# Performance work log

Measured on AMD Instinct MI355X. Metric: run time of the kernel, lower is better.

The kernel has to match this reference:

```python
import jax, jax.numpy as jnp
import numpy as np

L, B, S, CACHE = 2, 1, 2048, 2048
H, HKV, D, DM, FF, V = 16, 8, 128, 2048, 8192, 32000
EPS = 1e-6
ROPE_BASE = 10000.0


def setup_inputs() -> dict:
    key = jax.random.key(0)
    ks = jax.random.split(key, 18)
    std = 0.02
    r = lambda k, shape: (jax.random.normal(k, shape, dtype=jnp.float32) * std)
    return {
        "input_ids": jax.random.randint(ks[0], (B, S), 0, V),
        "embed": r(ks[1], (V, DM)),
        "Wq": r(ks[2], (L, DM, H * D)),
        "Wk": r(ks[3], (L, DM, HKV * D)),
        "Wv": r(ks[4], (L, DM, HKV * D)),
        "Wo": r(ks[5], (L, H * D, DM)),
        "Wg": r(ks[6], (L, DM, FF)),
        "Wu": r(ks[7], (L, DM, FF)),
        "Wd": r(ks[8], (L, FF, DM)),
        "ln1": jnp.ones((L, DM), jnp.float32),
        "ln2": jnp.ones((L, DM), jnp.float32),
        "final_norm": jnp.ones((DM,), jnp.float32),
        "lm_head": r(ks[9], (DM, V)),
        "k_cache": jax.random.normal(ks[10], (L, B, H, CACHE, D), jnp.float32),
        "v_cache": jax.random.normal(ks[11], (L, B, H, CACHE, D), jnp.float32),
    }


def rms_norm(x, w):
    return x * jax.lax.rsqrt(jnp.mean(x * x, axis=-1, keepdims=True) + EPS) * w


def apply_rope(x, pos):
    # x: [B,H,T,D], pos: [T]
    inv_freq = 1.0 / (ROPE_BASE ** (jnp.arange(0, D, 2, dtype=jnp.float32) / D))
    f = pos[:, None].astype(jnp.float32) * inv_freq[None, :]  # [T, D/2]
    emb = jnp.concatenate([f, f], axis=-1)                    # [T, D]
    cos, sin = jnp.cos(emb), jnp.sin(emb)
    rot = jnp.concatenate([-x[..., D // 2:], x[..., : D // 2]], axis=-1)
    return x * cos + rot * sin


def decoder_forward(input_ids, embed, Wq, Wk, Wv, Wo, Wg, Wu, Wd,
                    ln1, ln2, final_norm, lm_head, k_cache, v_cache):
    h = embed[input_ids]  # [B,S,DM]
    T = CACHE + S
    q_pos = jnp.arange(CACHE, CACHE + S)
    k_pos = jnp.arange(T)
    # causal mask: query i (global pos CACHE+i) attends keys <= CACHE+i
    mask = k_pos[None, :] <= (CACHE + jnp.arange(S))[:, None]  # [S,T]
    scale = 1.0 / np.sqrt(D)

    def layer(h, params):
        wq, wk, wv, wo, wg, wu, wd, l1, l2, kc, vc = params
        x = rms_norm(h, l1)
        q = (x @ wq).reshape(B, S, H, D).transpose(0, 2, 1, 3)     # [B,H,S,D]
        k = (x @ wk).reshape(B, S, HKV, D).transpose(0, 2, 1, 3)   # [B,HKV,S,D]
        v = (x @ wv).reshape(B, S, HKV, D).transpose(0, 2, 1, 3)
        k = jnp.repeat(k, H // HKV, axis=1)                        # repeat_kv
        v = jnp.repeat(v, H // HKV, axis=1)
        k = jnp.concatenate([kc, k], axis=2)                       # [B,H,T,D]
        v = jnp.concatenate([vc, v], axis=2)
        q = apply_rope(q, q_pos)
        k = apply_rope(k, k_pos)
        scores = jnp.einsum('bhqd,bhkd->bhqk', q, k) * scale
        scores = jnp.where(mask, scores, jnp.float32(-1e30))
        attn = jax.nn.softmax(scores, axis=-1)
        o = jnp.einsum('bhqk,bhkd->bhqd', attn, v)
        o = o.transpose(0, 2, 1, 3).reshape(B, S, H * D) @ wo
        h = h + o
        x = rms_norm(h, l2)
        h = h + (jax.nn.silu(x @ wg) * (x @ wu)) @ wd
        return h, None

    h, _ = jax.lax.scan(layer, h, (Wq, Wk, Wv, Wo, Wg, Wu, Wd, ln1, ln2, k_cache, v_cache))
    h = rms_norm(h, final_norm)
    return (h @ lm_head).astype(jnp.float32)  # logits [B,S,V]


def reference(input_ids, embed, Wq, Wk, Wv, Wo, Wg, Wu, Wd,
              ln1, ln2, final_norm, lm_head, k_cache, v_cache):
    return decoder_forward(input_ids, embed, Wq, Wk, Wv, Wo, Wg, Wu, Wd,
                           ln1, ln2, final_norm, lm_head, k_cache, v_cache)
```

## Files before the change

kernel.cpp:

```cpp
#include <hip/hip_runtime.h>

typedef __attribute__((ext_vector_type(8))) short bfrag8;
typedef __attribute__((ext_vector_type(4))) short bfrag4;
typedef __attribute__((ext_vector_type(4))) float facc4;

#define DEV_INLINE __device__ __forceinline__

DEV_INLINE short f2bf(float f) {
    union { float f; unsigned u; } x; x.f = f;
    unsigned r = (x.u + 0x7FFFu + ((x.u >> 16) & 1u)) >> 16;
    return (short)r;
}

DEV_INLINE float bf2f(short s) {
    union { unsigned u; float f; } x;
    x.u = ((unsigned)(unsigned short)s) << 16;
    return x.f;
}

DEV_INLINE unsigned pack_bf2(float a, float b) {
    return (unsigned)(unsigned short)f2bf(a) | ((unsigned)(unsigned short)f2bf(b) << 16);
}

#define GL2LDS(gp, lp) __builtin_amdgcn_global_load_lds( \
    (const __attribute__((address_space(1))) void*)(gp), \
    (__attribute__((address_space(3))) void*)(lp), 16, 0, 0)

#define MFMA16(a, b, c) __builtin_amdgcn_mfma_f32_16x16x32_bf16((a), (b), (c), 0, 0, 0)

__global__ __launch_bounds__(256) void embed_kernel(const int* __restrict__ ids,
                                                    const float* __restrict__ emb,
                                                    float* __restrict__ h) {
    int s = blockIdx.x;
    int id = ids[s];
    const float* src = emb + (size_t)id * 2048;
    float* dst = h + (size_t)s * 2048;
    int t = threadIdx.x;
    float4 a = *(const float4*)(src + t * 8);
    float4 b = *(const float4*)(src + t * 8 + 4);
    *(float4*)(dst + t * 8) = a;
    *(float4*)(dst + t * 8 + 4) = b;
}

__global__ __launch_bounds__(256) void rmsnorm_bf16_kernel(const float* __restrict__ in,
                                                           const float* __restrict__ w,
                                                           short* __restrict__ out) {
    int row = blockIdx.x;
    const float* x = in + (size_t)row * 2048;
    short* y = out + (size_t)row * 2048;
    int t = threadIdx.x;
    float4 a = *(const float4*)(x + t * 8);
    float4 b = *(const float4*)(x + t * 8 + 4);
    float ss = a.x*a.x + a.y*a.y + a.z*a.z + a.w*a.w
             + b.x*b.x + b.y*b.y + b.z*b.z + b.w*b.w;
#pragma unroll
    for (int off = 32; off >= 1; off >>= 1) ss += __shfl_xor(ss, off);
    __shared__ float red[4];
    if ((t & 63) == 0) red[t >> 6] = ss;
    __syncthreads();
    float tot = red[0] + red[1] + red[2] + red[3];
    float sc = rsqrtf(tot * (1.0f / 2048.0f) + 1e-6f);
    float4 wa = *(const float4*)(w + t * 8);
    float4 wb = *(const float4*)(w + t * 8 + 4);
    bfrag8 o;
    o[0] = f2bf(a.x * sc * wa.x); o[1] = f2bf(a.y * sc * wa.y);
    o[2] = f2bf(a.z * sc * wa.z); o[3] = f2bf(a.w * sc * wa.w);
    o[4] = f2bf(b.x * sc * wb.x); o[5] = f2bf(b.y * sc * wb.y);
    o[6] = f2bf(b.z * sc * wb.z); o[7] = f2bf(b.w * sc * wb.w);
    *(bfrag8*)(y + t * 8) = o;
}

__global__ __launch_bounds__(256) void wconv_kernel(const float* __restrict__ W,
                                                    short* __restrict__ Wt,
                                                    int K, int N) {
    __shared__ short Lt[64][72];
    int k0 = blockIdx.x * 64, n0 = blockIdx.y * 64;
    int tid = threadIdx.x;
    int r = tid >> 4, c = (tid & 15) * 4;
#pragma unroll
    for (int j = 0; j < 4; ++j) {
        int k = r + j * 16;
        float4 v = *(const float4*)(W + (size_t)(k0 + k) * N + n0 + c);
        Lt[c + 0][k] = f2bf(v.x); Lt[c + 1][k] = f2bf(v.y);
        Lt[c + 2][k] = f2bf(v.z); Lt[c + 3][k] = f2bf(v.w);
    }
    __syncthreads();
    int n = tid >> 3, kk = (tid & 7) * 8;
#pragma unroll
    for (int j = 0; j < 2; ++j)
        *(bfrag8*)(Wt + (size_t)(n0 + n + j * 32) * K + k0 + kk) = *(const bfrag8*)&Lt[n + j * 32][kk];
}

template<int OUT>
__global__ __launch_bounds__(512, 1) void gemmB(const short* __restrict__ A,
                                                const short* __restrict__ Bt,
                                                float* __restrict__ C,
                                                int K, int N) {
    constexpr int ASLOT = 256 * 64;
    constexpr int BOFF = 4 * ASLOT;
    __shared__ short lds[65536];
    char* ldsb = (char*)lds;
    int tid = threadIdx.x;
    int lane = tid & 63, wave = tid >> 6;
    int wm = wave >> 2, wn = wave & 3;
    int lr = lane & 15, lg = lane >> 4;

    int gx = gridDim.x;
    int nwg = gx * gridDim.y;
    int b = blockIdx.y * gx + blockIdx.x;
    int q8 = nwg >> 3, r8 = nwg & 7;
    int xcd = b & 7, idx = b >> 3;
    int lb = (xcd < r8) ? (xcd * (q8 + 1) + idx) : (r8 * (q8 + 1) + (xcd - r8) * q8 + idx);
    int bm = (lb % gx) * 256, bn = (lb / gx) * 256;

    facc4 acc[8][4];
#pragma unroll
    for (int m = 0; m < 8; ++m)
#pragma unroll
        for (int n = 0; n < 4; ++n) acc[m][n] = (facc4){0.f, 0.f, 0.f, 0.f};

    int rs = tid >> 2;
    int cs = (tid & 3) ^ ((rs >> 1) & 3);
    const size_t sK = (size_t)K;
    const short* Ag0 = A + (size_t)(bm + rs) * sK + cs * 8;
    const short* Ag1 = A + (size_t)(bm + rs + 128) * sK + cs * 8;
    const short* Bg0 = Bt + (size_t)(bn + rs) * sK + cs * 8;
    const short* Bg1 = Bt + (size_t)(bn + rs + 128) * sK + cs * 8;

    auto stage = [&](int u) {
        int sl = u & 3;
        int ko = u * 32;
        char* Ad = ldsb + sl * ASLOT + tid * 16;
        char* Bd = ldsb + BOFF + sl * ASLOT + tid * 16;
        GL2LDS(Ag0 + ko, Ad);
        GL2LDS(Ag1 + ko, Ad + 8192);
        GL2LDS(Bg0 + ko, Bd);
        GL2LDS(Bg1 + ko, Bd + 8192);
    };

    int NT = K >> 5;
    stage(0); stage(1); stage(2);

    int arow[8], brow[4];
#pragma unroll
    for (int m = 0; m < 8; ++m) arow[m] = wm * 128 + m * 16 + lr;
#pragma unroll
    for (int n = 0; n < 4; ++n) brow[n] = wn * 64 + n * 16 + lr;

    for (int t = 0; t < NT; ++t) {
        if (t < NT - 2)       asm volatile("s_waitcnt vmcnt(8)" ::: "memory");
        else if (t == NT - 2) asm volatile("s_waitcnt vmcnt(4)" ::: "memory");
        else                  asm volatile("s_waitcnt vmcnt(0)" ::: "memory");
        __builtin_amdgcn_s_barrier();
        __builtin_amdgcn_sched_barrier(0);
        const char* Ab = ldsb + (t & 3) * ASLOT;
        const char* Bb = ldsb + BOFF + (t & 3) * ASLOT;
        bfrag8 af[8], bf[4];
#pragma unroll
        for (int m = 0; m < 8; ++m) {
            int r = arow[m];
            af[m] = *(const bfrag8*)(Ab + r * 64 + ((lg ^ ((r >> 1) & 3)) << 4));
        }
#pragma unroll
        for (int n = 0; n < 4; ++n) {
            int r = brow[n];
            bf[n] = *(const bfrag8*)(Bb + r * 64 + ((lg ^ ((r >> 1) & 3)) << 4));
        }
        if (t + 3 < NT) stage(t + 3);
        __builtin_amdgcn_s_setprio(1);
#pragma unroll
        for (int m = 0; m < 8; ++m)
#pragma unroll
            for (int n = 0; n < 4; ++n)
                acc[m][n] = MFMA16(af[m], bf[n], acc[m][n]);
        __builtin_amdgcn_s_setprio(0);
    }

    int crow = bm + wm * 128 + lg * 4;
    int ccol = bn + wn * 64 + lr;
#pragma unroll
    for (int m = 0; m < 8; ++m)
#pragma unroll
        for (int n = 0; n < 4; ++n)
#pragma unroll
            for (int r = 0; r < 4; ++r) {
                size_t ci = (size_t)(crow + m * 16 + r) * N + ccol + n * 16;
                if constexpr (OUT == 0)      C[ci] = acc[m][n][r];
                else if constexpr (OUT == 1) C[ci] = C[ci] + acc[m][n][r];
                else                         ((short*)C)[ci] = f2bf(acc[m][n][r]);
            }
}

template<int OUT>
__global__ __launch_bounds__(256, 2) void gemmR(const short* __restrict__ A,
                                                const short* __restrict__ Bt,
                                                float* __restrict__ C,
                                                int K, int ldk, int N) {
    constexpr int ASLOT = 128 * 64;
    constexpr int BOFF = 4 * ASLOT;
    __shared__ short lds[4 * 256 * 32];
    char* ldsb = (char*)lds;
    int tid = threadIdx.x;
    int lane = tid & 63, wave = tid >> 6;
    int wm = wave >> 1, wn = wave & 1;
    int lr = lane & 15, lg = lane >> 4;

    int gx = gridDim.x;
    int nwg = gx * gridDim.y;
    int b = blockIdx.y * gx + blockIdx.x;
    int q8 = nwg >> 3, r8 = nwg & 7;
    int xcd = b & 7, idx = b >> 3;
    int lb = (xcd < r8) ? (xcd * (q8 + 1) + idx) : (r8 * (q8 + 1) + (xcd - r8) * q8 + idx);
    int bm = (lb % gx) * 128, bn = (lb / gx) * 128;

    facc4 acc[4][4];
#pragma unroll
    for (int m = 0; m < 4; ++m)
#pragma unroll
        for (int n = 0; n < 4; ++n) acc[m][n] = (facc4){0.f, 0.f, 0.f, 0.f};

    int rs = tid >> 2;
    int cs = (tid & 3) ^ ((rs >> 1) & 3);
    const size_t sK = (size_t)ldk;
    const short* Ag0 = A + (size_t)(bm + rs) * sK + cs * 8;
    const short* Ag1 = A + (size_t)(bm + rs + 64) * sK + cs * 8;
    const short* Bg0 = Bt + (size_t)(bn + rs) * sK + cs * 8;
    const short* Bg1 = Bt + (size_t)(bn + rs + 64) * sK + cs * 8;

    auto stage = [&](int u) {
        int sl = u & 3;
        int ko = u * 32;
        char* Ad = ldsb + sl * ASLOT + tid * 16;
        char* Bd = ldsb + BOFF + sl * ASLOT + tid * 16;
        GL2LDS(Ag0 + ko, Ad);
        GL2LDS(Ag1 + ko, Ad + 4096);
        GL2LDS(Bg0 + ko, Bd);
        GL2LDS(Bg1 + ko, Bd + 4096);
    };

    int NT = K >> 5;
    stage(0); stage(1); stage(2);

    int arow[4], brow[4];
#pragma unroll
    for (int m = 0; m < 4; ++m) arow[m] = wm * 64 + m * 16 + lr;
#pragma unroll
    for (int n = 0; n < 4; ++n) brow[n] = wn * 64 + n * 16 + lr;

    for (int t = 0; t < NT; ++t) {
        if (t < NT - 2)       asm volatile("s_waitcnt vmcnt(8)" ::: "memory");
        else if (t == NT - 2) asm volatile("s_waitcnt vmcnt(4)" ::: "memory");
        else                  asm volatile("s_waitcnt vmcnt(0)" ::: "memory");
        __builtin_amdgcn_s_barrier();
        __builtin_amdgcn_sched_barrier(0);
        const char* Ab = ldsb + (t & 3) * ASLOT;
        const char* Bb = ldsb + BOFF + (t & 3) * ASLOT;
        bfrag8 af[4], bf[4];
#pragma unroll
        for (int m = 0; m < 4; ++m) {
            int r = arow[m];
            af[m] = *(const bfrag8*)(Ab + r * 64 + ((lg ^ ((r >> 1) & 3)) << 4));
        }
#pragma unroll
        for (int n = 0; n < 4; ++n) {
            int r = brow[n];
            bf[n] = *(const bfrag8*)(Bb + r * 64 + ((lg ^ ((r >> 1) & 3)) << 4));
        }
        if (t + 3 < NT) stage(t + 3);
        __builtin_amdgcn_s_setprio(1);
#pragma unroll
        for (int m = 0; m < 4; ++m)
#pragma unroll
            for (int n = 0; n < 4; ++n)
                acc[m][n] = MFMA16(af[m], bf[n], acc[m][n]);
        __builtin_amdgcn_s_setprio(0);
    }

    int crow = bm + wm * 64 + lg * 4;
    int ccol = bn + wn * 64 + lr;
#pragma unroll
    for (int m = 0; m < 4; ++m)
#pragma unroll
        for (int n = 0; n < 4; ++n)
#pragma unroll
            for (int r = 0; r < 4; ++r) {
                size_t ci = (size_t)(crow + m * 16 + r) * N + ccol + n * 16;
                if constexpr (OUT == 0)      C[ci] = acc[m][n][r];
                else if constexpr (OUT == 1) C[ci] = C[ci] + acc[m][n][r];
                else                         ((short*)C)[ci] = f2bf(acc[m][n][r]);
            }
}

__global__ __launch_bounds__(256) void add2_kernel(float* __restrict__ h,
                                                   const float* __restrict__ p0,
                                                   const float* __restrict__ p1) {
    size_t i = ((size_t)blockIdx.x * 256 + threadIdx.x) * 4;
    float4 a = *(const float4*)(h + i);
    float4 x = *(const float4*)(p0 + i);
    float4 y = *(const float4*)(p1 + i);
    a.x += x.x + y.x; a.y += x.y + y.y; a.z += x.z + y.z; a.w += x.w + y.w;
    *(float4*)(h + i) = a;
}

#define ROPE_C 0.20762050593046010f
#define INV2PI 0.15915494309189535f
#define TWOPI  6.283185307179586f
#define QK_SCALE 0.08838834764831845f

DEV_INLINE void rope_sc(float pos, int j, float* s, float* c) {
    float f = pos * exp2f(-(float)j * ROPE_C);
    float r = f * INV2PI;
    r -= floorf(r);
    __sincosf(r * TWOPI, s, c);
}

__global__ __launch_bounds__(128) void prep_q_kernel(const float* __restrict__ qkv,
                                                     short* __restrict__ Qb) {
    int h = blockIdx.x, d = threadIdx.x;
    int s0 = blockIdx.y * 4;
#pragma unroll
    for (int i = 0; i < 4; ++i) {
        int s = s0 + i;
        const float* src = qkv + (size_t)s * 4096 + h * 128;
        float x = src[d], xp = src[d ^ 64];
        float sn, c;
        rope_sc((float)(2048 + s), d & 63, &sn, &c);
        float o = (d < 64) ? (x * c - xp * sn) : (x * c + xp * sn);
        Qb[((size_t)h * 2048 + s) * 128 + d] = f2bf(o * QK_SCALE);
    }
}

__global__ __launch_bounds__(128) void prep_k_kernel(const float* __restrict__ kc,
                                                     const float* __restrict__ qkv,
                                                     short* __restrict__ Kf) {
    int h = blockIdx.x, d = threadIdx.x;
    int t0 = blockIdx.y * 8;
#pragma unroll
    for (int i = 0; i < 8; ++i) {
        int t = t0 + i;
        float x, xp;
        if (t < 2048) {
            const float* src = kc + ((size_t)h * 2048 + t) * 128;
            x = src[d]; xp = src[d ^ 64];
        } else {
            const float* src = qkv + (size_t)(t - 2048) * 4096 + 2048 + (h >> 1) * 128;
            x = src[d]; xp = src[d ^ 64];
        }
        float sn, c;
        rope_sc((float)t, d & 63, &sn, &c);
        float o = (d < 64) ? (x * c - xp * sn) : (x * c + xp * sn);
        Kf[((size_t)h * 4096 + t) * 128 + d] = f2bf(o);
    }
}

__global__ __launch_bounds__(256) void prep_v_kernel(const float* __restrict__ vc,
                                                     const float* __restrict__ qkv,
                                                     short* __restrict__ Vt) {
    int h = blockIdx.x;
    int t0 = blockIdx.y * 64;
    __shared__ short Lt[128][72];
    int tid = threadIdx.x;
    int r = tid >> 2;
    int c0 = (tid & 3) * 32;
    int t = t0 + r;
    const float* src = (t < 2048)
        ? vc + ((size_t)h * 2048 + t) * 128 + c0
        : qkv + (size_t)(t - 2048) * 4096 + 3072 + (h >> 1) * 128 + c0;
#pragma unroll
    for (int i = 0; i < 32; i += 4) {
        float4 v = *(const float4*)(src + i);
        Lt[c0 + i + 0][r] = f2bf(v.x);
        Lt[c0 + i + 1][r] = f2bf(v.y);
        Lt[c0 + i + 2][r] = f2bf(v.z);
        Lt[c0 + i + 3][r] = f2bf(v.w);
    }
    __syncthreads();
    int d = tid >> 1;
    int hh = (tid & 1) * 32;
    short* dst = Vt + ((size_t)h * 128 + d) * 4096 + t0 + hh;
    const short* srcl = &Lt[d][hh];
#pragma unroll
    for (int i = 0; i < 32; i += 8)
        *(bfrag8*)(dst + i) = *(const bfrag8*)(srcl + i);
}

__global__ __launch_bounds__(256, 2) void attn_kernel(const short* __restrict__ Q,
                                                      const short* __restrict__ Kf,
                                                      const short* __restrict__ Vt,
                                                      float* __restrict__ Op,
                                                      float* __restrict__ Ml,
                                                      float* __restrict__ Ll) {
    int h = blockIdx.x;
    int qb = blockIdx.y * 64;
    int z = blockIdx.z;
    int tid = threadIdx.x;
    int lane = tid & 63, wave = tid >> 6;
    int lr = lane & 15, lg = lane >> 4;
    int qrow = qb + wave * 16;
    int qg = 2048 + qrow + lr;

    __shared__ short Ks[2][8192];
    __shared__ short Vs[2][8192];
    __shared__ short P[4][16][72];

    const short* kbase = Kf + (size_t)h * 4096 * 128;
    const short* vbase = Vt + (size_t)h * 128 * 4096;

    bfrag8 aq[4];
    {
        const short* qp = Q + ((size_t)h * 2048 + qrow + lr) * 128 + lg * 8;
#pragma unroll
        for (int dt = 0; dt < 4; ++dt) aq[dt] = *(const bfrag8*)(qp + dt * 32);
    }
    facc4 o[8];
#pragma unroll
    for (int n = 0; n < 8; ++n) o[n] = (facc4){0.f, 0.f, 0.f, 0.f};
    float m = -1e30f, l = 0.f;

    auto stage = [&](int buf, int t0) {
#pragma unroll
        for (int it = 0; it < 4; ++it) {
            int rk = it * 16 + (tid >> 4);
            int ck = (tid & 15) ^ (rk & 7);
            GL2LDS(kbase + (size_t)(t0 + rk) * 128 + ck * 8,
                   &Ks[buf][it * 2048 + tid * 8]);
            int rv = it * 32 + (tid >> 3);
            int cv = (tid & 7) ^ (rv & 7);
            GL2LDS(vbase + (size_t)rv * 4096 + t0 + cv * 8,
                   &Vs[buf][it * 2048 + tid * 8]);
        }
    };

    auto process = [&](int buf, int t0) {
        facc4 s[4];
#pragma unroll
        for (int j = 0; j < 4; ++j) {
            s[j] = (facc4){0.f, 0.f, 0.f, 0.f};
            int r = j * 16 + lr;
#pragma unroll
            for (int dt = 0; dt < 4; ++dt) {
                bfrag8 k = *(const bfrag8*)&Ks[buf][r * 128 + (((dt * 4 + lg) ^ (r & 7)) * 8)];
                s[j] = MFMA16(k, aq[dt], s[j]);
            }
        }
        float mx = m;
#pragma unroll
        for (int j = 0; j < 4; ++j)
#pragma unroll
            for (int r = 0; r < 4; ++r) {
                int ki = t0 + j * 16 + lg * 4 + r;
                if (ki > qg) s[j][r] = -1e30f;
                mx = fmaxf(mx, s[j][r]);
            }
        mx = fmaxf(mx, __shfl_xor(mx, 16));
        mx = fmaxf(mx, __shfl_xor(mx, 32));
        if (__any(mx > m + 8.f)) {
            float alpha = __expf(m - mx);
            m = mx;
            l *= alpha;
            float ab[4];
#pragma unroll
            for (int r = 0; r < 4; ++r) ab[r] = __shfl(alpha, lg * 4 + r);
#pragma unroll
            for (int n = 0; n < 8; ++n) {
                o[n][0] *= ab[0]; o[n][1] *= ab[1]; o[n][2] *= ab[2]; o[n][3] *= ab[3];
            }
        }
        float ps = 0.f;
#pragma unroll
        for (int j = 0; j < 4; ++j)
#pragma unroll
            for (int r = 0; r < 4; ++r) {
                s[j][r] = __expf(s[j][r] - m);
                ps += s[j][r];
            }
        ps += __shfl_xor(ps, 16);
        ps += __shfl_xor(ps, 32);
        l += ps;
        unsigned* prow = (unsigned*)&P[wave][lr][0];
#pragma unroll
        for (int j = 0; j < 4; ++j) {
            prow[j * 8 + lg * 2]     = pack_bf2(s[j][0], s[j][1]);
            prow[j * 8 + lg * 2 + 1] = pack_bf2(s[j][2], s[j][3]);
        }
        bfrag8 ap0 = *(const bfrag8*)&P[wave][lr][lg * 8];
        bfrag8 ap1 = *(const bfrag8*)&P[wave][lr][32 + lg * 8];
#pragma unroll
        for (int n = 0; n < 8; ++n) {
            int rv = n * 16 + lr;
            bfrag8 v0 = *(const bfrag8*)&Vs[buf][rv * 64 + (((lg) ^ (rv & 7)) * 8)];
            bfrag8 v1 = *(const bfrag8*)&Vs[buf][rv * 64 + (((4 + lg) ^ (rv & 7)) * 8)];
            o[n] = MFMA16(ap0, v0, o[n]);
            o[n] = MFMA16(ap1, v1, o[n]);
        }
    };

    int NT = (2048 + qb + 64) >> 6;
    int i0 = z ? (NT >> 1) : 0;
    int i1 = z ? NT : (NT >> 1);

    stage(0, i0 * 64);
    __syncthreads();
    int buf = 0;
    for (int i = i0; i < i1; ++i) {
        if (i + 1 < i1) stage(buf ^ 1, (i + 1) * 64);
        process(buf, i * 64);
        __syncthreads();
        buf ^= 1;
    }

#pragma unroll
    for (int n = 0; n < 8; ++n)
#pragma unroll
        for (int r = 0; r < 4; ++r)
            Op[(size_t)(z * 2048 + qrow + lg * 4 + r) * 2048 + h * 128 + n * 16 + lr] = o[n][r];
    if (lg == 0) {
        Ml[((size_t)z * 16 + h) * 2048 + qrow + lr] = m;
        Ll[((size_t)z * 16 + h) * 2048 + qrow + lr] = l;
    }
}

__global__ __launch_bounds__(256) void attn_combine(const float* __restrict__ Op,
                                                    const float* __restrict__ Ml,
                                                    const float* __restrict__ Ll,
                                                    short* __restrict__ Ob) {
    int row = blockIdx.x, t = threadIdx.x;
    int col0 = t * 8;
    int h = col0 >> 7;
    float m0 = Ml[(size_t)h * 2048 + row], m1 = Ml[(size_t)(16 + h) * 2048 + row];
    float l0 = Ll[(size_t)h * 2048 + row], l1 = Ll[(size_t)(16 + h) * 2048 + row];
    float mm = fmaxf(m0, m1);
    float a0 = __expf(m0 - mm), a1 = __expf(m1 - mm);
    float inv = 1.f / (l0 * a0 + l1 * a1);
    a0 *= inv; a1 *= inv;
    const float* p0 = Op + (size_t)row * 2048 + col0;
    const float* p1 = Op + (size_t)(2048 + row) * 2048 + col0;
    float4 x0 = *(const float4*)p0, x1 = *(const float4*)(p0 + 4);
    float4 y0 = *(const float4*)p1, y1 = *(const float4*)(p1 + 4);
    bfrag8 ov;
    ov[0] = f2bf(x0.x * a0 + y0.x * a1); ov[1] = f2bf(x0.y * a0 + y0.y * a1);
    ov[2] = f2bf(x0.z * a0 + y0.z * a1); ov[3] = f2bf(x0.w * a0 + y0.w * a1);
    ov[4] = f2bf(x1.x * a0 + y1.x * a1); ov[5] = f2bf(x1.y * a0 + y1.y * a1);
    ov[6] = f2bf(x1.z * a0 + y1.z * a1); ov[7] = f2bf(x1.w * a0 + y1.w * a1);
    *(bfrag8*)(Ob + (size_t)row * 2048 + col0) = ov;
}

__global__ __launch_bounds__(256) void silu_fused_kernel(const short* __restrict__ f,
                                                         short* __restrict__ out) {
    size_t v = (size_t)blockIdx.x * 256 + threadIdx.x;
    int r = (int)(v >> 10);
    int c = (int)(v & 1023) * 8;
    bfrag8 g = *(const bfrag8*)(f + (size_t)r * 16384 + c);
    bfrag8 u = *(const bfrag8*)(f + (size_t)r * 16384 + 8192 + c);
    bfrag8 o;
#pragma unroll
    for (int j = 0; j < 8; ++j) {
        float gf = bf2f(g[j]), uf = bf2f(u[j]);
        o[j] = f2bf(gf / (1.f + __expf(-gf)) * uf);
    }
    *(bfrag8*)(out + v * 8) = o;
}

extern "C" void kernel_launch(void* const* d_in, const int* in_sizes, int n_in,
                              void* d_out, int out_size, void* d_ws, size_t ws_size,
                              hipStream_t stream) {
    const int*   ids   = (const int*)d_in[0];
    const float* emb   = (const float*)d_in[1];
    const float* Wq    = (const float*)d_in[2];
    const float* Wk    = (const float*)d_in[3];
    const float* Wv    = (const float*)d_in[4];
    const float* Wo    = (const float*)d_in[5];
    const float* Wg    = (const float*)d_in[6];
    const float* Wu    = (const float*)d_in[7];
    const float* Wd    = (const float*)d_in[8];
    const float* ln1   = (const float*)d_in[9];
    const float* ln2   = (const float*)d_in[10];
    const float* fnorm = (const float*)d_in[11];
    const float* lmh   = (const float*)d_in[12];
    const float* kc    = (const float*)d_in[13];
    const float* vc    = (const float*)d_in[14];
    float* logits = (float*)d_out;

    char* ws = (char*)d_ws;
    float* hbuf   = (float*)(ws + ((size_t)0 << 20));
    short* xb     = (short*)(ws + ((size_t)16 << 20));
    float* qkvbuf = (float*)(ws + ((size_t)24 << 20));
    short* Ob     = (short*)(ws + ((size_t)56 << 20));
    short* wt     = (short*)(ws + ((size_t)64 << 20));
    short* Qb     = (short*)(ws + ((size_t)128 << 20));
    short* Kf     = (short*)(ws + ((size_t)136 << 20));
    short* Vt     = (short*)(ws + ((size_t)152 << 20));
    short* fbuf   = (short*)(ws + ((size_t)168 << 20));
    short* gb     = (short*)(ws + ((size_t)232 << 20));
    float* mlb    = (float*)(ws + ((size_t)264 << 20));
    float* Mlp    = mlb;
    float* Llp    = mlb + 2 * 16 * 2048;
    float* sk0    = qkvbuf;
    float* sk1    = qkvbuf + (size_t)4 * 1024 * 1024;
    short* lmwt   = (short*)(ws + ((size_t)64 << 20));

    embed_kernel<<<2048, 256, 0, stream>>>(ids, emb, hbuf);

    for (int l = 0; l < 2; ++l) {
        const float* wq  = Wq + (size_t)l * 2048 * 2048;
        const float* wk  = Wk + (size_t)l * 2048 * 1024;
        const float* wv  = Wv + (size_t)l * 2048 * 1024;
        const float* wo  = Wo + (size_t)l * 2048 * 2048;
        const float* wg  = Wg + (size_t)l * 2048 * 8192;
        const float* wu  = Wu + (size_t)l * 2048 * 8192;
        const float* wd  = Wd + (size_t)l * 8192 * 2048;
        const float* l1  = ln1 + (size_t)l * 2048;
        const float* l2  = ln2 + (size_t)l * 2048;
        const float* kcl = kc + (size_t)l * 16 * 2048 * 128;
        const float* vcl = vc + (size_t)l * 16 * 2048 * 128;

        rmsnorm_bf16_kernel<<<2048, 256, 0, stream>>>(hbuf, l1, xb);
        wconv_kernel<<<dim3(32, 32), 256, 0, stream>>>(wq, wt, 2048, 2048);
        wconv_kernel<<<dim3(32, 16), 256, 0, stream>>>(wk, wt + (size_t)2048 * 2048, 2048, 1024);
        wconv_kernel<<<dim3(32, 16), 256, 0, stream>>>(wv, wt + (size_t)3072 * 2048, 2048, 1024);
        gemmR<0><<<dim3(16, 32), 256, 0, stream>>>(xb, wt, qkvbuf, 2048, 2048, 4096);
        prep_q_kernel<<<dim3(16, 512), 128, 0, stream>>>(qkvbuf, Qb);
        prep_k_kernel<<<dim3(16, 512), 128, 0, stream>>>(kcl, qkvbuf, Kf);
        prep_v_kernel<<<dim3(16, 64), 256, 0, stream>>>(vcl, qkvbuf, Vt);
        attn_kernel<<<dim3(16, 32, 2), 256, 0, stream>>>(Qb, Kf, Vt, qkvbuf, Mlp, Llp);
        attn_combine<<<2048, 256, 0, stream>>>(qkvbuf, Mlp, Llp, Ob);
        wconv_kernel<<<dim3(32, 32), 256, 0, stream>>>(wo, wt, 2048, 2048);
        gemmR<1><<<dim3(16, 16), 256, 0, stream>>>(Ob, wt, hbuf, 2048, 2048, 2048);
        rmsnorm_bf16_kernel<<<2048, 256, 0, stream>>>(hbuf, l2, xb);
        wconv_kernel<<<dim3(32, 128), 256, 0, stream>>>(wg, wt, 2048, 8192);
        wconv_kernel<<<dim3(32, 128), 256, 0, stream>>>(wu, wt + (size_t)8192 * 2048, 2048, 8192);
        gemmB<2><<<dim3(8, 64), 512, 0, stream>>>(xb, wt, (float*)fbuf, 2048, 16384);
        silu_fused_kernel<<<8192, 256, 0, stream>>>(fbuf, gb);
        wconv_kernel<<<dim3(128, 32), 256, 0, stream>>>(wd, wt, 8192, 2048);
        gemmR<0><<<dim3(16, 16), 256, 0, stream>>>(gb, wt, sk0, 4096, 8192, 2048);
        gemmR<0><<<dim3(16, 16), 256, 0, stream>>>(gb + 4096, wt + 4096, sk1, 4096, 8192, 2048);
        add2_kernel<<<4096, 256, 0, stream>>>(hbuf, sk0, sk1);
    }
    rmsnorm_bf16_kernel<<<2048, 256, 0, stream>>>(hbuf, fnorm, xb);
    wconv_kernel<<<dim3(32, 500), 256, 0, stream>>>(lmh, lmwt, 2048, 32000);
    gemmB<0><<<dim3(8, 125), 512, 0, stream>>>(xb, lmwt, logits, 2048, 32000);
}
```

Before: 1.536 ms.

## Fuse SiLU-gating into gate/up GEMM epilogue and double query rows per attention block

```diff
diff --git a/kernel.cpp b/kernel.cpp
--- a/kernel.cpp
+++ b/kernel.cpp
@@ -70,6 +70,7 @@
     *(bfrag8*)(y + t * 8) = o;
 }
 
+template<int RMUL, int ROFF>
 __global__ __launch_bounds__(256) void wconv_kernel(const float* __restrict__ W,
                                                     short* __restrict__ Wt,
                                                     int K, int N) {
@@ -88,7 +89,8 @@
     int n = tid >> 3, kk = (tid & 7) * 8;
 #pragma unroll
     for (int j = 0; j < 2; ++j)
-        *(bfrag8*)(Wt + (size_t)(n0 + n + j * 32) * K + k0 + kk) = *(const bfrag8*)&Lt[n + j * 32][kk];
+        *(bfrag8*)(Wt + ((size_t)(n0 + n + j * 32) * RMUL + ROFF) * K + k0 + kk) =
+            *(const bfrag8*)&Lt[n + j * 32][kk];
 }
 
 template<int OUT>
@@ -184,10 +186,19 @@
         for (int n = 0; n < 4; ++n)
 #pragma unroll
             for (int r = 0; r < 4; ++r) {
-                size_t ci = (size_t)(crow + m * 16 + r) * N + ccol + n * 16;
-                if constexpr (OUT == 0)      C[ci] = acc[m][n][r];
-                else if constexpr (OUT == 1) C[ci] = C[ci] + acc[m][n][r];
-                else                         ((short*)C)[ci] = f2bf(acc[m][n][r]);
+                if constexpr (OUT == 3) {
+                    float v = acc[m][n][r];
+                    float p = __shfl_xor(v, 1);
+                    if ((lr & 1) == 0) {
+                        float res = v / (1.f + __expf(-v)) * p;
+                        size_t j = (size_t)((bn + wn * 64 + n * 16 + lr) >> 1);
+                        ((short*)C)[(size_t)(crow + m * 16 + r) * (N >> 1) + j] = f2bf(res);
+                    }
+                } else {
+                    size_t ci = (size_t)(crow + m * 16 + r) * N + ccol + n * 16;
+                    if constexpr (OUT == 0)      C[ci] = acc[m][n][r];
+                    else                         ((short*)C)[ci] = f2bf(acc[m][n][r]);
+                }
             }
 }
 
@@ -391,13 +402,15 @@
                                                       float* __restrict__ Ml,
                                                       float* __restrict__ Ll) {
     int h = blockIdx.x;
-    int qb = blockIdx.y * 64;
+    int qb = blockIdx.y * 128;
     int z = blockIdx.z;
     int tid = threadIdx.x;
     int lane = tid & 63, wave = tid >> 6;
     int lr = lane & 15, lg = lane >> 4;
-    int qrow = qb + wave * 16;
-    int qg = 2048 + qrow + lr;
+    int qrow0 = qb + wave * 16;
+    int qrow1 = qb + 64 + wave * 16;
+    int qg0 = 2048 + qrow0 + lr;
+    int qg1 = 2048 + qrow1 + lr;
 
     __shared__ short Ks[2][8192];
     __shared__ short Vs[2][8192];
@@ -406,16 +419,23 @@
     const short* kbase = Kf + (size_t)h * 4096 * 128;
     const short* vbase = Vt + (size_t)h * 128 * 4096;
 
-    bfrag8 aq[4];
+    bfrag8 aq0[4], aq1[4];
     {
-        const short* qp = Q + ((size_t)h * 2048 + qrow + lr) * 128 + lg * 8;
-#pragma unroll
-        for (int dt = 0; dt < 4; ++dt) aq[dt] = *(const bfrag8*)(qp + dt * 32);
-    }
-    facc4 o[8];
-#pragma unroll
-    for (int n = 0; n < 8; ++n) o[n] = (facc4){0.f, 0.f, 0.f, 0.f};
-    float m = -1e30f, l = 0.f;
+        const short* qp0 = Q + ((size_t)h * 2048 + qrow0 + lr) * 128 + lg * 8;
+        const short* qp1 = Q + ((size_t)h * 2048 + qrow1 + lr) * 128 + lg * 8;
+#pragma unroll
+        for (int dt = 0; dt < 4; ++dt) {
+            aq0[dt] = *(const bfrag8*)(qp0 + dt * 32);
+            aq1[dt] = *(const bfrag8*)(qp1 + dt * 32);
+        }
+    }
+    facc4 o0[8], o1[8];
+#pragma unroll
+    for (int n = 0; n < 8; ++n) {
+        o0[n] = (facc4){0.f, 0.f, 0.f, 0.f};
+        o1[n] = (facc4){0.f, 0.f, 0.f, 0.f};
+    }
+    float m0 = -1e30f, l0 = 0.f, m1 = -1e30f, l1 = 0.f;
 
     auto stage = [&](int buf, int t0) {
 #pragma unroll
@@ -431,7 +451,7 @@
         }
     };
 
-    auto process = [&](int buf, int t0) {
+    auto sgroup = [&](int buf, int t0, const bfrag8* aq, int qg, float& m, float& l, facc4* o) {
         facc4 s[4];
 #pragma unroll
         for (int j = 0; j < 4; ++j) {
@@ -495,7 +515,7 @@
         }
     };
 
-    int NT = (2048 + qb + 64) >> 6;
+    int NT = (2048 + qb + 128) >> 6;
     int i0 = z ? (NT >> 1) : 0;
     int i1 = z ? NT : (NT >> 1);
 
@@ -504,7 +524,8 @@
     int buf = 0;
     for (int i = i0; i < i1; ++i) {
         if (i + 1 < i1) stage(buf ^ 1, (i + 1) * 64);
-        process(buf, i * 64);
+        sgroup(buf, i * 64, aq0, qg0, m0, l0, o0);
+        sgroup(buf, i * 64, aq1, qg1, m1, l1, o1);
         __syncthreads();
         buf ^= 1;
     }
@@ -512,11 +533,15 @@
 #pragma unroll
     for (int n = 0; n < 8; ++n)
 #pragma unroll
-        for (int r = 0; r < 4; ++r)
-            Op[(size_t)(z * 2048 + qrow + lg * 4 + r) * 2048 + h * 128 + n * 16 + lr] = o[n][r];
+        for (int r = 0; r < 4; ++r) {
+            Op[(size_t)(z * 2048 + qrow0 + lg * 4 + r) * 2048 + h * 128 + n * 16 + lr] = o0[n][r];
+            Op[(size_t)(z * 2048 + qrow1 + lg * 4 + r) * 2048 + h * 128 + n * 16 + lr] = o1[n][r];
+        }
     if (lg == 0) {
-        Ml[((size_t)z * 16 + h) * 2048 + qrow + lr] = m;
-        Ll[((size_t)z * 16 + h) * 2048 + qrow + lr] = l;
+        Ml[((size_t)z * 16 + h) * 2048 + qrow0 + lr] = m0;
+        Ll[((size_t)z * 16 + h) * 2048 + qrow0 + lr] = l0;
+        Ml[((size_t)z * 16 + h) * 2048 + qrow1 + lr] = m1;
+        Ll[((size_t)z * 16 + h) * 2048 + qrow1 + lr] = l1;
     }
 }
 
@@ -545,22 +570,6 @@
     *(bfrag8*)(Ob + (size_t)row * 2048 + col0) = ov;
 }
 
-__global__ __launch_bounds__(256) void silu_fused_kernel(const short* __restrict__ f,
-                                                         short* __restrict__ out) {
-    size_t v = (size_t)blockIdx.x * 256 + threadIdx.x;
-    int r = (int)(v >> 10);
-    int c = (int)(v & 1023) * 8;
-    bfrag8 g = *(const bfrag8*)(f + (size_t)r * 16384 + c);
-    bfrag8 u = *(const bfrag8*)(f + (size_t)r * 16384 + 8192 + c);
-    bfrag8 o;
-#pragma unroll
-    for (int j = 0; j < 8; ++j) {
-        float gf = bf2f(g[j]), uf = bf2f(u[j]);
-        o[j] = f2bf(gf / (1.f + __expf(-gf)) * uf);
-    }
-    *(bfrag8*)(out + v * 8) = o;
-}
-
 extern "C" void kernel_launch(void* const* d_in, const int* in_sizes, int n_in,
                               void* d_out, int out_size, void* d_ws, size_t ws_size,
                               hipStream_t stream) {
@@ -590,9 +599,8 @@
     short* Qb     = (short*)(ws + ((size_t)128 << 20));
     short* Kf     = (short*)(ws + ((size_t)136 << 20));
     short* Vt     = (short*)(ws + ((size_t)152 << 20));
-    short* fbuf   = (short*)(ws + ((size_t)168 << 20));
-    short* gb     = (short*)(ws + ((size_t)232 << 20));
-    float* mlb    = (float*)(ws + ((size_t)264 << 20));
+    short* gb     = (short*)(ws + ((size_t)168 << 20));
+    float* mlb    = (float*)(ws + ((size_t)200 << 20));
     float* Mlp    = mlb;
     float* Llp    = mlb + 2 * 16 * 2048;
     float* sk0    = qkvbuf;
@@ -615,28 +623,27 @@
         const float* vcl = vc + (size_t)l * 16 * 2048 * 128;
 
         rmsnorm_bf16_kernel<<<2048, 256, 0, stream>>>(hbuf, l1, xb);
-        wconv_kernel<<<dim3(32, 32), 256, 0, stream>>>(wq, wt, 2048, 2048);
-        wconv_kernel<<<dim3(32, 16), 256, 0, stream>>>(wk, wt + (size_t)2048 * 2048, 2048, 1024);
-        wconv_kernel<<<dim3(32, 16), 256, 0, stream>>>(wv, wt + (size_t)3072 * 2048, 2048, 1024);
+        wconv_kernel<1, 0><<<dim3(32, 32), 256, 0, stream>>>(wq, wt, 2048, 2048);
+        wconv_kernel<1, 0><<<dim3(32, 16), 256, 0, stream>>>(wk, wt + (size_t)2048 * 2048, 2048, 1024);
+        wconv_kernel<1, 0><<<dim3(32, 16), 256, 0, stream>>>(wv, wt + (size_t)3072 * 2048, 2048, 1024);
         gemmR<0><<<dim3(16, 32), 256, 0, stream>>>(xb, wt, qkvbuf, 2048, 2048, 4096);
         prep_q_kernel<<<dim3(16, 512), 128, 0, stream>>>(qkvbuf, Qb);
         prep_k_kernel<<<dim3(16, 512), 128, 0, stream>>>(kcl, qkvbuf, Kf);
         prep_v_kernel<<<dim3(16, 64), 256, 0, stream>>>(vcl, qkvbuf, Vt);
-        attn_kernel<<<dim3(16, 32, 2), 256, 0, stream>>>(Qb, Kf, Vt, qkvbuf, Mlp, Llp);
+        attn_kernel<<<dim3(16, 16, 2), 256, 0, stream>>>(Qb, Kf, Vt, qkvbuf, Mlp, Llp);
         attn_combine<<<2048, 256, 0, stream>>>(qkvbuf, Mlp, Llp, Ob);
-        wconv_kernel<<<dim3(32, 32), 256, 0, stream>>>(wo, wt, 2048, 2048);
+        wconv_kernel<1, 0><<<dim3(32, 32), 256, 0, stream>>>(wo, wt, 2048, 2048);
         gemmR<1><<<dim3(16, 16), 256, 0, stream>>>(Ob, wt, hbuf, 2048, 2048, 2048);
         rmsnorm_bf16_kernel<<<2048, 256, 0, stream>>>(hbuf, l2, xb);
-        wconv_kernel<<<dim3(32, 128), 256, 0, stream>>>(wg, wt, 2048, 8192);
-        wconv_kernel<<<dim3(32, 128), 256, 0, stream>>>(wu, wt + (size_t)8192 * 2048, 2048, 8192);
-        gemmB<2><<<dim3(8, 64), 512, 0, stream>>>(xb, wt, (float*)fbuf, 2048, 16384);
-        silu_fused_kernel<<<8192, 256, 0, stream>>>(fbuf, gb);
-        wconv_kernel<<<dim3(128, 32), 256, 0, stream>>>(wd, wt, 8192, 2048);
+        wconv_kernel<2, 0><<<dim3(32, 128), 256, 0, stream>>>(wg, wt, 2048, 8192);
+        wconv_kernel<2, 1><<<dim3(32, 128), 256, 0, stream>>>(wu, wt, 2048, 8192);
+        gemmB<3><<<dim3(8, 64), 512, 0, stream>>>(xb, wt, (float*)gb, 2048, 16384);
+        wconv_kernel<1, 0><<<dim3(128, 32), 256, 0, stream>>>(wd, wt, 8192, 2048);
         gemmR<0><<<dim3(16, 16), 256, 0, stream>>>(gb, wt, sk0, 4096, 8192, 2048);
         gemmR<0><<<dim3(16, 16), 256, 0, stream>>>(gb + 4096, wt + 4096, sk1, 4096, 8192, 2048);
         add2_kernel<<<4096, 256, 0, stream>>>(hbuf, sk0, sk1);
     }
     rmsnorm_bf16_kernel<<<2048, 256, 0, stream>>>(hbuf, fnorm, xb);
-    wconv_kernel<<<dim3(32, 500), 256, 0, stream>>>(lmh, lmwt, 2048, 32000);
+    wconv_kernel<1, 0><<<dim3(32, 500), 256, 0, stream>>>(lmh, lmwt, 2048, 32000);
     gemmB<0><<<dim3(8, 125), 512, 0, stream>>>(xb, lmwt, logits, 2048, 32000);
 }
```

Measured after the change: 1.587 ms. 1.03x slower.
